# Optimization experiments

Measured on AMD Instinct MI355X. Metric: run time of the kernel, lower is better.

## Reference

```python
import jax, jax.numpy as jnp
import numpy as np

B, S, DIN = 4, 2048, 1024
H, D = 16, 64  # num_head, per-head dim_out


def _xavier(key, shape):
    fan_in, fan_out = shape[0], shape[1]
    limit = float(np.sqrt(6.0 / (fan_in + fan_out)))
    return jax.random.uniform(key, shape, jnp.float32, -limit, limit)


def setup_inputs() -> dict:
    key = jax.random.key(0)
    k_x, k_q, k_k, k_v, k_o = jax.random.split(key, 5)
    inputs = jax.random.normal(k_x, (B, S, DIN), jnp.float32)
    # weights stored as [in, out] (transpose of torch Linear.weight); bias zeros
    return {
        "inputs": inputs,
        "wq": _xavier(k_q, (DIN, H * D)), "bq": jnp.zeros((H * D,), jnp.float32),
        "wk": _xavier(k_k, (DIN, H * D)), "bk": jnp.zeros((H * D,), jnp.float32),
        "wv": _xavier(k_v, (DIN, H * D)), "bv": jnp.zeros((H * D,), jnp.float32),
        "wo": _xavier(k_o, (H * D, D)),  "bo": jnp.zeros((D,), jnp.float32),
    }


def reference(inputs, wq, bq, wk, bk, wv, bv, wo, bo):
    b, s, _ = inputs.shape
    q = (inputs @ wq + bq).reshape(b, s, H, D).transpose(0, 2, 1, 3)  # bhsd
    k = (inputs @ wk + bk).reshape(b, s, H, D).transpose(0, 2, 1, 3)
    v = (inputs @ wv + bv).reshape(b, s, H, D).transpose(0, 2, 1, 3)
    scores = jnp.einsum('bhsd,bhSd->bhsS', q, k) / jnp.sqrt(jnp.float32(D))
    p = jax.nn.softmax(scores, axis=-1)
    o = jnp.einsum('bhsS,bhSd->bhsd', p, v)
    o = o.transpose(0, 2, 1, 3).reshape(b, s, H * D)
    return o @ wo + bo  # [b, s, D]
```

## Files before the change

### kernel.cpp

```cpp
#include <hip/hip_runtime.h>

typedef __attribute__((ext_vector_type(8))) __bf16 bf16x8;
typedef __attribute__((ext_vector_type(4))) float f32x4;

#define NB   4
#define NS   2048
#define NDIN 1024
#define NH   16
#define ND   64
#define NHD  1024
#define NM   (NB * NS)

__device__ __forceinline__ float bf2f(unsigned short u) {
    unsigned int x = ((unsigned int)u) << 16;
    return __builtin_bit_cast(float, x);
}
__device__ __forceinline__ unsigned short f2bf(float f) {
    unsigned int u = __builtin_bit_cast(unsigned int, f);
    u += 0x7fff + ((u >> 16) & 1);
    return (unsigned short)(u >> 16);
}
__device__ __forceinline__ unsigned int cvt_pk_bf16(float lo, float hi) {
    unsigned int r;
    asm("v_cvt_pk_bf16_f32 %0, %1, %2" : "=v"(r) : "v"(lo), "v"(hi));
    return r;
}
__device__ __forceinline__ void gload16(const unsigned short* g, unsigned short* l) {
    __builtin_amdgcn_global_load_lds((const __attribute__((address_space(1))) unsigned int*)g,
                                     (__attribute__((address_space(3))) unsigned int*)l, 16, 0, 0);
}

__global__ __launch_bounds__(256) void prep(
    const float* __restrict__ X, const float* __restrict__ wq,
    const float* __restrict__ wk, const float* __restrict__ wv,
    const float* __restrict__ wo, unsigned short* __restrict__ Xb,
    unsigned short* __restrict__ Wt, unsigned short* __restrict__ WoT) {
    __shared__ unsigned short t[32][33];
    int blk = blockIdx.x, tid = threadIdx.x;
    if (blk < 4096) {
        int i = blk * 256 + tid;
        float4 a = ((const float4*)X)[i * 2];
        float4 b = ((const float4*)X)[i * 2 + 1];
        union { uint4 u; unsigned short s[8]; } o;
        o.s[0] = f2bf(a.x); o.s[1] = f2bf(a.y); o.s[2] = f2bf(a.z); o.s[3] = f2bf(a.w);
        o.s[4] = f2bf(b.x); o.s[5] = f2bf(b.y); o.s[6] = f2bf(b.z); o.s[7] = f2bf(b.w);
        *(uint4*)(Xb + (size_t)i * 8) = o.u;
    } else if (blk < 4096 + 3072) {
        int bb = blk - 4096;
        int z = bb >> 10, rem = bb & 1023;
        const float* src = z == 0 ? wq : z == 1 ? wk : wv;
        unsigned short* dst = Wt + (size_t)z * 1024 * 1024;
        int k0 = (rem & 31) * 32, n0 = (rem >> 5) * 32;
        int tx = tid & 31, ty = tid >> 5;
#pragma unroll
        for (int i = 0; i < 32; i += 8)
            t[ty + i][tx] = f2bf(src[(size_t)(k0 + ty + i) * 1024 + (n0 + tx)]);
        __syncthreads();
#pragma unroll
        for (int i = 0; i < 32; i += 8)
            dst[(size_t)(n0 + ty + i) * 1024 + (k0 + tx)] = t[tx][ty + i];
    } else {
        int bb = blk - 7168;
        int k0 = (bb & 31) * 32, n0 = (bb >> 5) * 32;
        int tx = tid & 31, ty = tid >> 5;
#pragma unroll
        for (int i = 0; i < 32; i += 8)
            t[ty + i][tx] = f2bf(wo[(size_t)(k0 + ty + i) * 64 + (n0 + tx)]);
        __syncthreads();
#pragma unroll
        for (int i = 0; i < 32; i += 8)
            WoT[(size_t)(n0 + ty + i) * 1024 + (k0 + tx)] = t[tx][ty + i];
    }
}

__global__ __launch_bounds__(256) void gemm_qkv(
    const unsigned short* __restrict__ X, const unsigned short* __restrict__ Wt,
    const float* __restrict__ bq, const float* __restrict__ bk,
    const float* __restrict__ bv,
    unsigned short* __restrict__ Q, unsigned short* __restrict__ K,
    unsigned short* __restrict__ V) {
    __shared__ unsigned short smem[16384];

    int lin = blockIdx.x;
    int xcd = lin & 7, ii = lin >> 3;
    int mt = xcd * 8 + (ii & 7);
    int nt = ii >> 3;
    int mb = mt * 128, nb = nt * 128;

    int tid = threadIdx.x;
    int wid = tid >> 6, lane = tid & 63, quad = lane >> 4, l16 = lane & 15;
    int wm = (wid & 1) * 64, wn = (wid >> 1) * 64;

    int srow = 16 * wid + (lane >> 2);
    int scol = (lane & 3) * 8;
    const unsigned short* pa0 = X + (size_t)(mb + srow) * NDIN + scol;
    const unsigned short* pa1 = pa0 + (size_t)64 * NDIN;
    const unsigned short* pb0 = Wt + (size_t)(nb + srow) * NDIN + scol;
    const unsigned short* pb1 = pb0 + (size_t)64 * NDIN;

    auto stage = [&](int buf) {
        unsigned short* la = smem + buf * 8192 + wid * 512;
        unsigned short* lb = smem + buf * 8192 + 4096 + wid * 512;
        gload16(pa0, la);
        gload16(pa1, la + 2048);
        gload16(pb0, lb);
        gload16(pb1, lb + 2048);
        pa0 += 32; pa1 += 32; pb0 += 32; pb1 += 32;
    };

    f32x4 acc[4][4];
#pragma unroll
    for (int i = 0; i < 4; i++)
#pragma unroll
        for (int j = 0; j < 4; j++) acc[i][j] = (f32x4){0.f, 0.f, 0.f, 0.f};

    stage(0);
    __syncthreads();
    int cur = 0;
    for (int k0 = 0; k0 < NDIN; k0 += 32) {
        if (k0 + 32 < NDIN) stage(cur ^ 1);
        const unsigned short* Ab = smem + cur * 8192;
        const unsigned short* Bb = Ab + 4096;
        bf16x8 af[4], bfr[4];
#pragma unroll
        for (int i = 0; i < 4; i++)
            af[i] = *(const bf16x8*)(Ab + (wm + i * 16 + l16) * 32 + quad * 8);
#pragma unroll
        for (int j = 0; j < 4; j++)
            bfr[j] = *(const bf16x8*)(Bb + (wn + j * 16 + l16) * 32 + quad * 8);
#pragma unroll
        for (int i = 0; i < 4; i++)
#pragma unroll
            for (int j = 0; j < 4; j++)
                acc[i][j] = __builtin_amdgcn_mfma_f32_16x16x32_bf16(af[i], bfr[j], acc[i][j], 0, 0, 0);
        __syncthreads();
        cur ^= 1;
    }

    unsigned short (*Cl)[128] = (unsigned short (*)[128])smem;
    int wsel = nb >> 10;
    if (wsel < 2) {
        const float* bias = (wsel == 0) ? bq : bk;
        unsigned short* dstp = (wsel == 0) ? Q : K;
#pragma unroll
        for (int i = 0; i < 4; i++)
#pragma unroll
            for (int j = 0; j < 4; j++) {
                int nl = wn + j * 16 + l16;
                float bias_v = bias[(nb & 1023) + nl];
#pragma unroll
                for (int r = 0; r < 4; r++) {
                    int ml = wm + i * 16 + quad * 4 + r;
                    int pc = ((nl >> 3) ^ (ml & 15));
                    Cl[ml][(pc << 3) | (nl & 7)] = f2bf(acc[i][j][r] + bias_v);
                }
            }
        __syncthreads();
        int hl = tid >> 7, sl = tid & 127;
        int h = ((nb & 1023) >> 6) + hl;
        int m = mb + sl, b = m >> 11, sidx = m & 2047;
        unsigned short* orow = dstp + ((size_t)((b * NH + h) * NS + sidx)) * ND;
#pragma unroll
        for (int c = 0; c < 8; c++) {
            int pc = ((hl * 8 + c) ^ (sl & 15));
            *(uint4*)(orow + c * 8) = *(const uint4*)(&Cl[sl][pc << 3]);
        }
    } else {
#pragma unroll
        for (int i = 0; i < 4; i++)
#pragma unroll
            for (int j = 0; j < 4; j++) {
                int nl = wn + j * 16 + l16;
                float bias_v = bv[(nb & 1023) + nl];
#pragma unroll
                for (int r = 0; r < 4; r++) {
                    int pml = wm + (i >> 1) * 32 + quad * 8 + (i & 1) * 4 + r;
                    int pc = ((pml >> 3) ^ (nl & 15));
                    Cl[nl][(pc << 3) | (pml & 7)] = f2bf(acc[i][j][r] + bias_v);
                }
            }
        __syncthreads();
        int b = mb >> 11, smb = mb & 2047;
        int h0 = (nb & 1023) >> 6;
#pragma unroll
        for (int c = 0; c < 8; c++) {
            int o = c * 256 + tid;
            int row = o >> 4, sc = o & 15;
            int pc = sc ^ (row & 15);
            uint4 v = *(const uint4*)(&Cl[row][pc << 3]);
            int h = h0 + (row >> 6), d = row & 63;
            *(uint4*)(V + ((size_t)((b * NH + h) * ND + d)) * NS + smb + sc * 8) = v;
        }
    }
}

__global__ __launch_bounds__(256, 2) void attn(
    const unsigned short* __restrict__ Q, const unsigned short* __restrict__ K,
    const unsigned short* __restrict__ VT, unsigned short* __restrict__ Obuf) {
    __shared__ unsigned short Kl[2][64][64];
    __shared__ unsigned short Vt[2][64][64];

    int lin = blockIdx.x;
    int xcd = lin & 7, idx = lin >> 3;
    int bh = ((idx >> 3) << 3) | xcd;
    int qt = idx & 7;

    size_t base = (size_t)bh * NS * ND;
    int tid = threadIdx.x, wid = tid >> 6, lane = tid & 63;
    int quad = lane >> 4, l16 = lane & 15;
    int lx = l16 & 7;
    int q0 = qt * 256 + wid * 64;

    bf16x8 qa[4][2];
#pragma unroll
    for (int s = 0; s < 4; s++)
#pragma unroll
        for (int f = 0; f < 2; f++) {
            union { uint4 u; unsigned short sv[8]; } in_, out_;
            in_.u = *(const uint4*)(Q + base + (size_t)(q0 + s * 16 + l16) * ND + f * 32 + quad * 8);
#pragma unroll
            for (int j = 0; j < 8; j++) out_.sv[j] = f2bf(bf2f(in_.sv[j]) * 0.125f);
            qa[s][f] = __builtin_bit_cast(bf16x8, out_.u);
        }

    float lrow[4] = {0.f, 0.f, 0.f, 0.f};
    f32x4 o[4][4];
#pragma unroll
    for (int s = 0; s < 4; s++)
#pragma unroll
        for (int t = 0; t < 4; t++) o[s][t] = (f32x4){0.f, 0.f, 0.f, 0.f};

    int r0 = wid * 16 + (lane >> 3), r1 = r0 + 8;
    int p0 = lane & 7;
    const unsigned short* kp0 = K + base + (size_t)r0 * ND + ((p0 ^ (r0 & 7)) * 8);
    const unsigned short* kp1 = K + base + (size_t)r1 * ND + ((p0 ^ (r1 & 7)) * 8);
    const unsigned short* vp0 = VT + base + (size_t)r0 * NS + ((p0 ^ (r0 & 7)) * 8);
    const unsigned short* vp1 = VT + base + (size_t)r1 * NS + ((p0 ^ (r1 & 7)) * 8);

    auto stageKV = [&](int buf) {
        unsigned short* kb = &Kl[buf][0][0] + wid * 1024;
        unsigned short* vb = &Vt[buf][0][0] + wid * 1024;
        gload16(kp0, kb);
        gload16(kp1, kb + 512);
        gload16(vp0, vb);
        gload16(vp1, vb + 512);
    };

    stageKV(0);
    __syncthreads();

    int cur = 0;
    for (int kc = 0; kc < NS; kc += 64) {
        bool more = (kc + 64 < NS);
        if (more) {
            kp0 += 64 * ND; kp1 += 64 * ND; vp0 += 64; vp1 += 64;
            stageKV(cur ^ 1);
        }

        bf16x8 kb[4][2], vb[4][2];
#pragma unroll
        for (int u = 0; u < 4; u++) {
            const unsigned short* kr = &Kl[cur][u * 16 + l16][0];
            kb[u][0] = *(const bf16x8*)(kr + ((quad ^ lx) << 3));
            kb[u][1] = *(const bf16x8*)(kr + (((4 + quad) ^ lx) << 3));
            const unsigned short* vr = &Vt[cur][u * 16 + l16][0];
            vb[u][0] = *(const bf16x8*)(vr + ((quad ^ lx) << 3));
            vb[u][1] = *(const bf16x8*)(vr + (((4 + quad) ^ lx) << 3));
        }

#pragma unroll
        for (int s = 0; s < 4; s++) {
            f32x4 st[4];
            __builtin_amdgcn_s_setprio(1);
#pragma unroll
            for (int sub = 0; sub < 4; sub++) {
                f32x4 c = (f32x4){0.f, 0.f, 0.f, 0.f};
                c = __builtin_amdgcn_mfma_f32_16x16x32_bf16(kb[sub][0], qa[s][0], c, 0, 0, 0);
                c = __builtin_amdgcn_mfma_f32_16x16x32_bf16(kb[sub][1], qa[s][1], c, 0, 0, 0);
                st[sub] = c;
            }
            __builtin_amdgcn_s_setprio(0);

            float sum = 0.f;
#pragma unroll
            for (int sub = 0; sub < 4; sub++)
#pragma unroll
                for (int r = 0; r < 4; r++) {
                    float pv = __expf(st[sub][r]);
                    st[sub][r] = pv;
                    sum += pv;
                }
            lrow[s] += sum;
            unsigned int a0 = cvt_pk_bf16(st[0][0], st[0][1]);
            unsigned int a1 = cvt_pk_bf16(st[0][2], st[0][3]);
            unsigned int a2 = cvt_pk_bf16(st[1][0], st[1][1]);
            unsigned int a3 = cvt_pk_bf16(st[1][2], st[1][3]);
            bf16x8 pb0 = __builtin_bit_cast(bf16x8, (uint4){a0, a1, a2, a3});
            unsigned int b0 = cvt_pk_bf16(st[2][0], st[2][1]);
            unsigned int b1 = cvt_pk_bf16(st[2][2], st[2][3]);
            unsigned int b2 = cvt_pk_bf16(st[3][0], st[3][1]);
            unsigned int b3 = cvt_pk_bf16(st[3][2], st[3][3]);
            bf16x8 pb1 = __builtin_bit_cast(bf16x8, (uint4){b0, b1, b2, b3});

            __builtin_amdgcn_s_setprio(1);
#pragma unroll
            for (int t = 0; t < 4; t++) {
                o[s][t] = __builtin_amdgcn_mfma_f32_16x16x32_bf16(vb[t][0], pb0, o[s][t], 0, 0, 0);
                o[s][t] = __builtin_amdgcn_mfma_f32_16x16x32_bf16(vb[t][1], pb1, o[s][t], 0, 0, 0);
            }
            __builtin_amdgcn_s_setprio(0);
        }

        __syncthreads();
        cur ^= 1;
    }

    int b = bh >> 4, h = bh & 15;
#pragma unroll
    for (int s = 0; s < 4; s++) {
        float ls = lrow[s];
        ls += __shfl_xor(ls, 16, 64);
        ls += __shfl_xor(ls, 32, 64);
        float inv = 1.0f / ls;
        int q = q0 + s * 16 + l16;
#pragma unroll
        for (int t = 0; t < 4; t++) {
            uint2 w;
            w.x = cvt_pk_bf16(o[s][t][0] * inv, o[s][t][1] * inv);
            w.y = cvt_pk_bf16(o[s][t][2] * inv, o[s][t][3] * inv);
            *(uint2*)(Obuf + (size_t)(b * NS + q) * NHD + h * ND + t * 16 + quad * 4) = w;
        }
    }
}

__global__ __launch_bounds__(256) void out_proj(
    const unsigned short* __restrict__ Obuf, const unsigned short* __restrict__ WoT,
    const float* __restrict__ bo, float* __restrict__ Out) {
    __shared__ float red[4][16][64];
    int m0 = blockIdx.x * 16;
    int tid = threadIdx.x, wid = tid >> 6, lane = tid & 63;
    int quad = lane >> 4, l16 = lane & 15;
    f32x4 acc[4];
#pragma unroll
    for (int t = 0; t < 4; t++) acc[t] = (f32x4){0.f, 0.f, 0.f, 0.f};
    int kb = wid * 256;
    for (int k0 = kb; k0 < kb + 256; k0 += 32) {
        bf16x8 a = *(const bf16x8*)(Obuf + (size_t)(m0 + l16) * NHD + k0 + quad * 8);
#pragma unroll
        for (int t = 0; t < 4; t++) {
            bf16x8 b = *(const bf16x8*)(WoT + (size_t)(t * 16 + l16) * NHD + k0 + quad * 8);
            acc[t] = __builtin_amdgcn_mfma_f32_16x16x32_bf16(a, b, acc[t], 0, 0, 0);
        }
    }
#pragma unroll
    for (int t = 0; t < 4; t++)
#pragma unroll
        for (int r = 0; r < 4; r++) red[wid][t * 4 + r][lane] = acc[t][r];
    __syncthreads();
    if (tid < 64) {
        int q2 = tid >> 4, s16 = tid & 15;
#pragma unroll
        for (int t = 0; t < 4; t++) {
            int n = t * 16 + s16;
            float bb = bo[n];
#pragma unroll
            for (int r = 0; r < 4; r++) {
                int idx = t * 4 + r;
                float v = red[0][idx][tid] + red[1][idx][tid] + red[2][idx][tid] + red[3][idx][tid];
                int m = m0 + q2 * 4 + r;
                Out[(size_t)m * ND + n] = v + bb;
            }
        }
    }
}

extern "C" void kernel_launch(void* const* d_in, const int* in_sizes, int n_in,
                              void* d_out, int out_size, void* d_ws, size_t ws_size,
                              hipStream_t stream) {
    const float* X  = (const float*)d_in[0];
    const float* wq = (const float*)d_in[1];
    const float* bq = (const float*)d_in[2];
    const float* wk = (const float*)d_in[3];
    const float* bk = (const float*)d_in[4];
    const float* wv = (const float*)d_in[5];
    const float* bv = (const float*)d_in[6];
    const float* wo = (const float*)d_in[7];
    const float* bo = (const float*)d_in[8];
    float* Out = (float*)d_out;

    char* w = (char*)d_ws;
    unsigned short* Wt  = (unsigned short*)w; w += (size_t)3072 * 1024 * 2;
    unsigned short* WoT = (unsigned short*)w; w += (size_t)64 * 1024 * 2;
    unsigned short* Xb  = (unsigned short*)w; w += (size_t)NM * NDIN * 2;
    unsigned short* Qb  = (unsigned short*)w; w += (size_t)NM * NHD * 2;
    unsigned short* Kb  = (unsigned short*)w; w += (size_t)NM * NHD * 2;
    unsigned short* Vb  = (unsigned short*)w; w += (size_t)NM * NHD * 2;
    unsigned short* Ob  = (unsigned short*)w; w += (size_t)NM * NHD * 2;

    prep<<<7232, 256, 0, stream>>>(X, wq, wk, wv, wo, Xb, Wt, WoT);
    gemm_qkv<<<1536, 256, 0, stream>>>(Xb, Wt, bq, bk, bv, Qb, Kb, Vb);
    attn<<<512, 256, 0, stream>>>(Qb, Kb, Vb, Ob);
    out_proj<<<512, 256, 0, stream>>>(Ob, WoT, bo, Out);
}
```

Before: 247.4 us.

## Double KV tile to 128 keys per iteration and read K/V fragments from LDS inline

Raises the attention KV chunk from 64 to 128 keys per loop iteration, with larger double-buffered LDS tiles and a new swizzled load mapping for K and V^T. This halves the number of barriers and loop iterations. K and V fragments are now read from LDS inside the MFMA loops instead of being preloaded into registers, which cuts register pressure. The cost is redundant LDS reads across the four query sub-tiles and 64KB of LDS per block, which may limit occupancy.

```diff
diff --git a/kernel.cpp b/kernel.cpp
--- a/kernel.cpp
+++ b/kernel.cpp
@@ -197,8 +197,8 @@
 __global__ __launch_bounds__(256, 2) void attn(
     const unsigned short* __restrict__ Q, const unsigned short* __restrict__ K,
     const unsigned short* __restrict__ VT, unsigned short* __restrict__ Obuf) {
-    __shared__ unsigned short Kl[2][64][64];
-    __shared__ unsigned short Vt[2][64][64];
+    __shared__ unsigned short Kl[2][128][64];
+    __shared__ unsigned short Vt[2][64][128];
 
     int lin = blockIdx.x;
     int xcd = lin & 7, idx = lin >> 3;
@@ -230,60 +230,55 @@
 #pragma unroll
         for (int t = 0; t < 4; t++) o[s][t] = (f32x4){0.f, 0.f, 0.f, 0.f};
 
-    int r0 = wid * 16 + (lane >> 3), r1 = r0 + 8;
-    int p0 = lane & 7;
-    const unsigned short* kp0 = K + base + (size_t)r0 * ND + ((p0 ^ (r0 & 7)) * 8);
-    const unsigned short* kp1 = K + base + (size_t)r1 * ND + ((p0 ^ (r1 & 7)) * 8);
-    const unsigned short* vp0 = VT + base + (size_t)r0 * NS + ((p0 ^ (r0 & 7)) * 8);
-    const unsigned short* vp1 = VT + base + (size_t)r1 * NS + ((p0 ^ (r1 & 7)) * 8);
+    int krA = wid * 32 + (lane >> 3), kcA = lane & 7;
+    int vrA = wid * 16 + (lane >> 4), vcA = lane & 15;
+    const unsigned short* kpg = K + base + (size_t)krA * ND + ((kcA ^ (krA & 7)) * 8);
+    const unsigned short* vpgE = VT + base + (size_t)vrA * NS
+                               + ((((vcA & 7) ^ ((vrA + 0) & 7)) | (vcA & 8)) * 8);
+    const unsigned short* vpgO = VT + base + (size_t)vrA * NS
+                               + ((((vcA & 7) ^ ((vrA + 4) & 7)) | (vcA & 8)) * 8);
 
     auto stageKV = [&](int buf) {
-        unsigned short* kb = &Kl[buf][0][0] + wid * 1024;
-        unsigned short* vb = &Vt[buf][0][0] + wid * 1024;
-        gload16(kp0, kb);
-        gload16(kp1, kb + 512);
-        gload16(vp0, vb);
-        gload16(vp1, vb + 512);
+        unsigned short* kb = &Kl[buf][0][0] + wid * 2048;
+        unsigned short* vb = &Vt[buf][0][0] + wid * 2048;
+#pragma unroll
+        for (int i = 0; i < 4; i++) gload16(kpg + (size_t)i * 8 * ND, kb + i * 512);
+        gload16(vpgE + (size_t)0 * 4 * NS, vb + 0 * 512);
+        gload16(vpgO + (size_t)1 * 4 * NS, vb + 1 * 512);
+        gload16(vpgE + (size_t)2 * 4 * NS, vb + 2 * 512);
+        gload16(vpgO + (size_t)3 * 4 * NS, vb + 3 * 512);
     };
 
     stageKV(0);
     __syncthreads();
 
     int cur = 0;
-    for (int kc = 0; kc < NS; kc += 64) {
-        bool more = (kc + 64 < NS);
+    for (int kc = 0; kc < NS; kc += 128) {
+        bool more = (kc + 128 < NS);
         if (more) {
-            kp0 += 64 * ND; kp1 += 64 * ND; vp0 += 64; vp1 += 64;
+            kpg += 128 * ND; vpgE += 128; vpgO += 128;
             stageKV(cur ^ 1);
         }
 
-        bf16x8 kb[4][2], vb[4][2];
-#pragma unroll
-        for (int u = 0; u < 4; u++) {
-            const unsigned short* kr = &Kl[cur][u * 16 + l16][0];
-            kb[u][0] = *(const bf16x8*)(kr + ((quad ^ lx) << 3));
-            kb[u][1] = *(const bf16x8*)(kr + (((4 + quad) ^ lx) << 3));
-            const unsigned short* vr = &Vt[cur][u * 16 + l16][0];
-            vb[u][0] = *(const bf16x8*)(vr + ((quad ^ lx) << 3));
-            vb[u][1] = *(const bf16x8*)(vr + (((4 + quad) ^ lx) << 3));
-        }
-
 #pragma unroll
         for (int s = 0; s < 4; s++) {
-            f32x4 st[4];
+            f32x4 st[8];
             __builtin_amdgcn_s_setprio(1);
 #pragma unroll
-            for (int sub = 0; sub < 4; sub++) {
+            for (int sub = 0; sub < 8; sub++) {
+                const unsigned short* kr = &Kl[cur][sub * 16 + l16][0];
+                bf16x8 kb0 = *(const bf16x8*)(kr + ((quad ^ lx) << 3));
+                bf16x8 kb1 = *(const bf16x8*)(kr + (((4 + quad) ^ lx) << 3));
                 f32x4 c = (f32x4){0.f, 0.f, 0.f, 0.f};
-                c = __builtin_amdgcn_mfma_f32_16x16x32_bf16(kb[sub][0], qa[s][0], c, 0, 0, 0);
-                c = __builtin_amdgcn_mfma_f32_16x16x32_bf16(kb[sub][1], qa[s][1], c, 0, 0, 0);
+                c = __builtin_amdgcn_mfma_f32_16x16x32_bf16(kb0, qa[s][0], c, 0, 0, 0);
+                c = __builtin_amdgcn_mfma_f32_16x16x32_bf16(kb1, qa[s][1], c, 0, 0, 0);
                 st[sub] = c;
             }
             __builtin_amdgcn_s_setprio(0);
 
             float sum = 0.f;
 #pragma unroll
-            for (int sub = 0; sub < 4; sub++)
+            for (int sub = 0; sub < 8; sub++)
 #pragma unroll
                 for (int r = 0; r < 4; r++) {
                     float pv = __expf(st[sub][r]);
@@ -301,12 +296,29 @@
             unsigned int b2 = cvt_pk_bf16(st[3][0], st[3][1]);
             unsigned int b3 = cvt_pk_bf16(st[3][2], st[3][3]);
             bf16x8 pb1 = __builtin_bit_cast(bf16x8, (uint4){b0, b1, b2, b3});
+            unsigned int c0 = cvt_pk_bf16(st[4][0], st[4][1]);
+            unsigned int c1 = cvt_pk_bf16(st[4][2], st[4][3]);
+            unsigned int c2 = cvt_pk_bf16(st[5][0], st[5][1]);
+            unsigned int c3 = cvt_pk_bf16(st[5][2], st[5][3]);
+            bf16x8 pb2 = __builtin_bit_cast(bf16x8, (uint4){c0, c1, c2, c3});
+            unsigned int d0 = cvt_pk_bf16(st[6][0], st[6][1]);
+            unsigned int d1 = cvt_pk_bf16(st[6][2], st[6][3]);
+            unsigned int d2 = cvt_pk_bf16(st[7][0], st[7][1]);
+            unsigned int d3 = cvt_pk_bf16(st[7][2], st[7][3]);
+            bf16x8 pb3 = __builtin_bit_cast(bf16x8, (uint4){d0, d1, d2, d3});
 
             __builtin_amdgcn_s_setprio(1);
 #pragma unroll
             for (int t = 0; t < 4; t++) {
-                o[s][t] = __builtin_amdgcn_mfma_f32_16x16x32_bf16(vb[t][0], pb0, o[s][t], 0, 0, 0);
-                o[s][t] = __builtin_amdgcn_mfma_f32_16x16x32_bf16(vb[t][1], pb1, o[s][t], 0, 0, 0);
+                const unsigned short* vr = &Vt[cur][t * 16 + l16][0];
+                bf16x8 vb0 = *(const bf16x8*)(vr + ((quad ^ lx) << 3));
+                bf16x8 vb1 = *(const bf16x8*)(vr + (((4 + quad) ^ lx) << 3));
+                bf16x8 vb2 = *(const bf16x8*)(vr + 64 + ((quad ^ lx) << 3));
+                bf16x8 vb3 = *(const bf16x8*)(vr + 64 + (((4 + quad) ^ lx) << 3));
+                o[s][t] = __builtin_amdgcn_mfma_f32_16x16x32_bf16(vb0, pb0, o[s][t], 0, 0, 0);
+                o[s][t] = __builtin_amdgcn_mfma_f32_16x16x32_bf16(vb1, pb1, o[s][t], 0, 0, 0);
+                o[s][t] = __builtin_amdgcn_mfma_f32_16x16x32_bf16(vb2, pb2, o[s][t], 0, 0, 0);
+                o[s][t] = __builtin_amdgcn_mfma_f32_16x16x32_bf16(vb3, pb3, o[s][t], 0, 0, 0);
             }
             __builtin_amdgcn_s_setprio(0);
         }
```

Result: no change. 249.1 us (+0.7%).
